# Performance work log

Measured on AMD Instinct MI355X. Metric: run time of the kernel, lower is better.

The kernel has to match this reference:

```python
import jax, jax.numpy as jnp
import numpy as np

NEG = float(-2**32 + 1)  # mask fill value used by the original module
H = 8  # number of heads (matches init kwarg h)


def setup_inputs() -> dict:
    key = jax.random.key(0)
    B, S, D, Q, V = 4, 2048, 512, 64, 64
    ks = jax.random.split(key, 10)
    sc = 1.0 / np.sqrt(D)
    x = jax.random.normal(ks[0], (B, S, D), jnp.float32)
    padding_mask = jax.random.randint(ks[1], (B, S), 0, 2, jnp.int32)
    Wq = jax.random.normal(ks[2], (H * Q, D), jnp.float32) * sc
    bq = jnp.zeros((H * Q,), jnp.float32)
    Wk = jax.random.normal(ks[3], (H * Q, D), jnp.float32) * sc
    bk = jnp.zeros((H * Q,), jnp.float32)
    Wv = jax.random.normal(ks[4], (H * V, D), jnp.float32) * sc
    bv = jnp.zeros((H * V,), jnp.float32)
    Wo = jax.random.normal(ks[5], (D, H * V), jnp.float32) * (1.0 / np.sqrt(H * V))
    bo = jnp.zeros((D,), jnp.float32)
    return {"x": x, "padding_mask": padding_mask, "Wq": Wq, "bq": bq,
            "Wk": Wk, "bk": bk, "Wv": Wv, "bv": bv, "Wo": Wo, "bo": bo}


def reference(x, padding_mask, Wq, bq, Wk, bk, Wv, bv, Wo, bo):
    # stage is hardcoded to 'train' (mask=True in init), so the causal branch runs.
    B, S, D = x.shape
    q_dim = Wq.shape[0] // H
    v_dim = Wv.shape[0] // H

    def split_heads(t, d):
        # torch: cat(chunk(h, dim=-1), dim=0) -> head-major [H*B, S, d]
        return t.reshape(B, S, H, d).transpose(2, 0, 1, 3).reshape(H * B, S, d)

    Qh = split_heads(x @ Wq.T + bq, q_dim)   # [H*B, S, q]
    Kh = split_heads(x @ Wk.T + bk, q_dim)
    Vh = split_heads(x @ Wv.T + bv, v_dim)

    score = jnp.einsum('nsd,ntd->nst', Qh, Kh) / jnp.sqrt(jnp.float32(q_dim))  # [H*B,S,S]
    pre_score = score  # module returns the UNMASKED scores (saved before masking)

    # causal mask (mask=True, stage=='train')
    causal = jnp.tril(jnp.ones((S, S), jnp.float32))
    score = jnp.where(causal > 0, score, NEG)

    # padding mask: built batch-major [B*H,S,S] while score is head-major [H*B,...]
    # -- faithful reproduction of the original ordering quirk.
    pm = jnp.broadcast_to(padding_mask[:, None, None, :], (B, H, S, S)).reshape(B * H, S, S)
    score = jnp.where(pm == 0, NEG, score)

    attn = jax.nn.softmax(score, axis=-1)
    out = jnp.einsum('nst,ntd->nsd', attn, Vh)  # [H*B, S, v]

    # torch: cat(chunk(h, dim=0), dim=-1) -> [B, S, H*v]
    heads = out.reshape(H, B, S, v_dim).transpose(1, 2, 0, 3).reshape(B, S, H * v_dim)
    self_attention = heads @ Wo.T + bo
    return self_attention, pre_score
```

## Files before the change

### kernel.cpp

```cpp
#include <hip/hip_runtime.h>
#include <hip/hip_fp16.h>
#include <math.h>

typedef _Float16 f16;
typedef _Float16 f16x8 __attribute__((ext_vector_type(8)));
typedef _Float16 f16x4 __attribute__((ext_vector_type(4)));
typedef float    f32x4 __attribute__((ext_vector_type(4)));

#define MFMA16(a,b,c) __builtin_amdgcn_mfma_f32_16x16x32_f16(a, b, c, 0, 0, 0)

#define MASKNEG (-6.0e9f)
#define DEADTHR (-1.0e9f)
#define LOG2E   1.44269504088896f

__global__ __launch_bounds__(256) void qkv_gemm(
    const float* __restrict__ x,
    const float* __restrict__ Wq, const float* __restrict__ bq,
    const float* __restrict__ Wk, const float* __restrict__ bk,
    const float* __restrict__ Wv, const float* __restrict__ bv,
    f16* __restrict__ Qws, f16* __restrict__ Kws, f16* __restrict__ Vt)
{
    __shared__ f16 Al[128 * 48];
    __shared__ f16 Wl[64 * 48];

    const int tid = threadIdx.x;
    const int bx  = blockIdx.x;
    const int m0  = blockIdx.y * 128;
    const int widx = bx >> 3;
    const int n0   = (bx & 7) * 64;

    const float* W    = (widx == 0) ? Wq : (widx == 1) ? Wk : Wv;
    const float* bias = (widx == 0) ? bq : (widx == 1) ? bk : bv;
    const float scl  = (widx == 0) ? 0.125f : 1.0f;

    const int wid = tid >> 6, lane = tid & 63;
    const int g = lane >> 4, c = lane & 15;
    const int wm = (wid >> 1) * 64, wn = (wid & 1) * 32;
    const int sr = tid >> 3, sc = tid & 7;

    f32x4 acc[4][2] = {};

    for (int kk = 0; kk < 512; kk += 32) {
        __syncthreads();
        #pragma unroll
        for (int rr = 0; rr < 4; ++rr) {
            int row = sr + rr * 32;
            float4 v = *(const float4*)&x[(size_t)(m0 + row) * 512 + kk + sc * 4];
            f16x4 h4 = {(f16)v.x, (f16)v.y, (f16)v.z, (f16)v.w};
            *(f16x4*)&Al[row * 48 + sc * 4] = h4;
        }
        #pragma unroll
        for (int rr = 0; rr < 2; ++rr) {
            int row = sr + rr * 32;
            float4 v = *(const float4*)&W[(size_t)(n0 + row) * 512 + kk + sc * 4];
            f16x4 h4 = {(f16)v.x, (f16)v.y, (f16)v.z, (f16)v.w};
            *(f16x4*)&Wl[row * 48 + sc * 4] = h4;
        }
        __syncthreads();

        f16x8 b0 = *(const f16x8*)&Wl[(wn +  0 + c) * 48 + g * 8];
        f16x8 b1 = *(const f16x8*)&Wl[(wn + 16 + c) * 48 + g * 8];
        #pragma unroll
        for (int mf = 0; mf < 4; ++mf) {
            f16x8 a = *(const f16x8*)&Al[(wm + mf * 16 + c) * 48 + g * 8];
            acc[mf][0] = MFMA16(a, b0, acc[mf][0]);
            acc[mf][1] = MFMA16(a, b1, acc[mf][1]);
        }
    }

    #pragma unroll
    for (int nf = 0; nf < 2; ++nf) {
        int cc = n0 + wn + nf * 16 + c;
        float bval = bias[cc];
        #pragma unroll
        for (int mf = 0; mf < 4; ++mf) {
            if (widx < 2) {
                f16* outp = (widx == 0) ? Qws : Kws;
                #pragma unroll
                for (int r = 0; r < 4; ++r) {
                    int mrow = m0 + wm + mf * 16 + g * 4 + r;
                    outp[(size_t)mrow * 512 + cc] = (f16)((acc[mf][nf][r] + bval) * scl);
                }
            } else {
                int h  = n0 >> 6;
                int d  = wn + nf * 16 + c;
                int t0 = m0 + wm + mf * 16 + g * 4;
                int b  = t0 >> 11;
                int ts = t0 & 2047;
                int nn = h * 4 + b;
                f16x4 pk = {(f16)(acc[mf][nf][0] + bval), (f16)(acc[mf][nf][1] + bval),
                            (f16)(acc[mf][nf][2] + bval), (f16)(acc[mf][nf][3] + bval)};
                *(f16x4*)&Vt[((size_t)(nn * 64 + d)) * 2048 + ts] = pk;
            }
        }
    }
}

__global__ __launch_bounds__(256) void vsum_kernel(
    const f16* __restrict__ Vt, float* __restrict__ Vsum)
{
    const int row  = blockIdx.x * 4 + (threadIdx.x >> 6);
    const int lane = threadIdx.x & 63;
    const f16* p = Vt + (size_t)row * 2048;
    float s = 0.f;
    #pragma unroll
    for (int i = 0; i < 4; ++i) {
        f16x8 v = *(const f16x8*)&p[i * 512 + lane * 8];
        #pragma unroll
        for (int j = 0; j < 8; ++j) s += (float)v[j];
    }
    #pragma unroll
    for (int off = 1; off < 64; off <<= 1) s += __shfl_xor(s, off, 64);
    if (lane == 0) Vsum[row] = s;
}

__global__ __launch_bounds__(256) void attn_kernel(
    const f16* __restrict__ Qws, const f16* __restrict__ Kws,
    const f16* __restrict__ Vt,  const int* __restrict__ pmask,
    const float* __restrict__ Vsum,
    float* __restrict__ pre_score, f16* __restrict__ attn_out)
{
    __shared__ f16 Kl[64 * 72];
    __shared__ f16 Vl[64 * 72];
    __shared__ f16 Pl[4][32 * 72];
    __shared__ float Bias[2048];

    const int tid = threadIdx.x;
    const int wid = tid >> 6, lane = tid & 63;
    const int g = lane >> 4, c = lane & 15;
    const int qt = blockIdx.x;
    const int n  = blockIdx.y;
    const int h = n >> 2, b = n & 3;
    const int pmrow = n >> 3;
    const int qlo = qt * 64 + wid * 16;
    const int qhi = (31 - qt) * 64 + wid * 16;
    const int qrel = wid * 16 + c;

    {
        const int i0 = tid * 8;
        const int4* p4 = (const int4*)(pmask + pmrow * 2048 + i0);
        int4 m0 = p4[0], m1 = p4[1];
        Bias[i0 + 0] = m0.x ? 0.f : MASKNEG;
        Bias[i0 + 1] = m0.y ? 0.f : MASKNEG;
        Bias[i0 + 2] = m0.z ? 0.f : MASKNEG;
        Bias[i0 + 3] = m0.w ? 0.f : MASKNEG;
        Bias[i0 + 4] = m1.x ? 0.f : MASKNEG;
        Bias[i0 + 5] = m1.y ? 0.f : MASKNEG;
        Bias[i0 + 6] = m1.z ? 0.f : MASKNEG;
        Bias[i0 + 7] = m1.w ? 0.f : MASKNEG;
    }

    f16x8 qf[2][2];
    #pragma unroll
    for (int ks = 0; ks < 2; ++ks) {
        qf[0][ks] = *(const f16x8*)
            &Qws[(size_t)(b * 2048 + qlo + c) * 512 + h * 64 + ks * 32 + g * 8];
        qf[1][ks] = *(const f16x8*)
            &Qws[(size_t)(b * 2048 + qhi + c) * 512 + h * 64 + ks * 32 + g * 8];
    }

    f32x4 o[2][4] = {};
    float mrow[2] = {-INFINITY, -INFINITY};
    float lrow[2] = {0.f, 0.f};

    const int sr = tid >> 3, sc = tid & 7;
    const f16* Kbase = Kws + (size_t)(b * 2048) * 512 + h * 64;
    const f16* Vbase = Vt + (size_t)(n * 64) * 2048;
    float* prow0 = pre_score + ((size_t)n * 2048 + qlo + c) * 2048;
    float* prow1 = pre_score + ((size_t)n * 2048 + qhi + c) * 2048;

    const int stageEnd = 32 - qt;

    uint4 ka0, ka1, va0, va1;
    auto glbload = [&](int kt) {
        ka0 = *(const uint4*)&Kbase[(size_t)(kt * 64 + sr) * 512 + sc * 8];
        ka1 = *(const uint4*)&Kbase[(size_t)(kt * 64 + sr + 32) * 512 + sc * 8];
        va0 = *(const uint4*)&Vbase[(size_t)sr * 2048 + kt * 64 + sc * 8];
        va1 = *(const uint4*)&Vbase[(size_t)(sr + 32) * 2048 + kt * 64 + sc * 8];
    };

    glbload(0);
    for (int kt = 0; kt < stageEnd; ++kt) {
        asm volatile("s_waitcnt lgkmcnt(0)" ::: "memory");
        __builtin_amdgcn_s_barrier();
        *(uint4*)&Kl[sr * 72 + sc * 8]        = ka0;
        *(uint4*)&Kl[(sr + 32) * 72 + sc * 8] = ka1;
        *(uint4*)&Vl[sr * 72 + sc * 8]        = va0;
        *(uint4*)&Vl[(sr + 32) * 72 + sc * 8] = va1;
        asm volatile("s_waitcnt lgkmcnt(0)" ::: "memory");
        __builtin_amdgcn_s_barrier();
        if (kt + 1 < stageEnd) glbload(kt + 1);

        f32x4 s2[2][4] = {};
        #pragma unroll
        for (int kc = 0; kc < 4; ++kc)
            #pragma unroll
            for (int ks = 0; ks < 2; ++ks) {
                f16x8 kf = *(const f16x8*)&Kl[(kc * 16 + c) * 72 + ks * 32 + g * 8];
                s2[0][kc] = MFMA16(kf, qf[0][ks], s2[0][kc]);
                s2[1][kc] = MFMA16(kf, qf[1][ks], s2[1][kc]);
            }

        #pragma unroll
        for (int kc = 0; kc < 4; ++kc) {
            *(f32x4*)&prow0[kt * 64 + kc * 16 + g * 4] = s2[0][kc];
            *(f32x4*)&prow1[kt * 64 + kc * 16 + g * 4] = s2[1][kc];
        }

        f32x4 bi[4];
        #pragma unroll
        for (int kc = 0; kc < 4; ++kc)
            bi[kc] = *(const f32x4*)&Bias[kt * 64 + kc * 16 + g * 4];

        const bool L0 = (kt <= qt);
        const bool bnd0 = (kt == qt), bnd1 = (kt == 31 - qt);

        #pragma unroll
        for (int mi = 0; mi < 2; ++mi) {
            if (mi == 0 && !L0) continue;
            const bool bnd = mi ? bnd1 : bnd0;
            float sl[4][4];
            #pragma unroll
            for (int kc = 0; kc < 4; ++kc)
                #pragma unroll
                for (int r = 0; r < 4; ++r) {
                    float sv = s2[mi][kc][r] + bi[kc][r];
                    int klocal = kc * 16 + g * 4 + r;
                    sl[kc][r] = (bnd && klocal > qrel) ? MASKNEG : sv;
                }
            float rm = sl[0][0];
            #pragma unroll
            for (int kc = 0; kc < 4; ++kc)
                #pragma unroll
                for (int r = 0; r < 4; ++r) rm = fmaxf(rm, sl[kc][r]);
            rm = fmaxf(rm, __shfl_xor(rm, 16, 64));
            rm = fmaxf(rm, __shfl_xor(rm, 32, 64));
            float mn = fmaxf(mrow[mi], rm);
            float alpha = exp2f((mrow[mi] - mn) * LOG2E);
            mrow[mi] = mn;
            float ml2 = mn * LOG2E;
            float rs = 0.f;
            #pragma unroll
            for (int kc = 0; kc < 4; ++kc) {
                f16x4 pk;
                #pragma unroll
                for (int r = 0; r < 4; ++r) {
                    float p = exp2f(fmaf(sl[kc][r], LOG2E, -ml2));
                    rs += p;
                    pk[r] = (f16)p;
                }
                *(f16x4*)&Pl[wid][(mi * 16 + c) * 72 + kc * 16 + g * 4] = pk;
            }
            rs += __shfl_xor(rs, 16, 64);
            rs += __shfl_xor(rs, 32, 64);
            lrow[mi] = lrow[mi] * alpha + rs;
            #pragma unroll
            for (int r = 0; r < 4; ++r) {
                float af = __shfl(alpha, g * 4 + r, 64);
                #pragma unroll
                for (int dn = 0; dn < 4; ++dn) o[mi][dn][r] *= af;
            }
        }
        asm volatile("s_waitcnt lgkmcnt(0)" ::: "memory");

        #pragma unroll
        for (int ks = 0; ks < 2; ++ks) {
            f16x8 pa0, pa1;
            if (L0) pa0 = *(const f16x8*)&Pl[wid][( 0 + c) * 72 + ks * 32 + g * 8];
            pa1 = *(const f16x8*)&Pl[wid][(16 + c) * 72 + ks * 32 + g * 8];
            #pragma unroll
            for (int dn = 0; dn < 4; ++dn) {
                f16x8 vb = *(const f16x8*)&Vl[(dn * 16 + c) * 72 + ks * 32 + g * 8];
                if (L0) o[0][dn] = MFMA16(pa0, vb, o[0][dn]);
                o[1][dn] = MFMA16(pa1, vb, o[1][dn]);
            }
        }
    }

    for (int kt = stageEnd; kt < 32; ++kt) {
        f32x4 s2[2][4] = {};
        #pragma unroll
        for (int kc = 0; kc < 4; ++kc)
            #pragma unroll
            for (int ks = 0; ks < 2; ++ks) {
                f16x8 kf = *(const f16x8*)
                    &Kbase[(size_t)(kt * 64 + kc * 16 + c) * 512 + ks * 32 + g * 8];
                s2[0][kc] = MFMA16(kf, qf[0][ks], s2[0][kc]);
                s2[1][kc] = MFMA16(kf, qf[1][ks], s2[1][kc]);
            }
        #pragma unroll
        for (int kc = 0; kc < 4; ++kc) {
            *(f32x4*)&prow0[kt * 64 + kc * 16 + g * 4] = s2[0][kc];
            *(f32x4*)&prow1[kt * 64 + kc * 16 + g * 4] = s2[1][kc];
        }
    }

    #pragma unroll
    for (int mi = 0; mi < 2; ++mi) {
        int qb = mi ? qhi : qlo;
        #pragma unroll
        for (int r = 0; r < 4; ++r) {
            float lo = __shfl(lrow[mi], g * 4 + r, 64);
            float mo = __shfl(mrow[mi], g * 4 + r, 64);
            int srow = qb + g * 4 + r;
            bool dead = (mo < DEADTHR);
            float inv_l = dead ? 0.f : 1.0f / lo;
            #pragma unroll
            for (int dn = 0; dn < 4; ++dn) {
                float val = dead ? Vsum[n * 64 + dn * 16 + c] * (1.0f / 2048.0f)
                                 : o[mi][dn][r] * inv_l;
                attn_out[(size_t)(b * 2048 + srow) * 512 + h * 64 + dn * 16 + c] = (f16)val;
            }
        }
    }
}

__global__ __launch_bounds__(256) void out_gemm(
    const f16* __restrict__ Aattn, const float* __restrict__ Wo,
    const float* __restrict__ bo, float* __restrict__ outp)
{
    __shared__ f16 Al[128 * 48];
    __shared__ f16 Wl[64 * 48];

    const int tid = threadIdx.x;
    const int n0 = blockIdx.x * 64;
    const int m0 = blockIdx.y * 128;
    const int wid = tid >> 6, lane = tid & 63;
    const int g = lane >> 4, c = lane & 15;
    const int wm = (wid >> 1) * 64, wn = (wid & 1) * 32;

    const int sr4 = tid >> 2, sc4 = tid & 3;
    const int sr8 = tid >> 3, sc8 = tid & 7;

    f32x4 acc[4][2] = {};

    for (int kk = 0; kk < 512; kk += 32) {
        __syncthreads();
        #pragma unroll
        for (int rr = 0; rr < 2; ++rr) {
            int row = sr4 + rr * 64;
            *(uint4*)&Al[row * 48 + sc4 * 8] =
                *(const uint4*)&Aattn[(size_t)(m0 + row) * 512 + kk + sc4 * 8];
        }
        #pragma unroll
        for (int rr = 0; rr < 2; ++rr) {
            int row = sr8 + rr * 32;
            float4 v = *(const float4*)&Wo[(size_t)(n0 + row) * 512 + kk + sc8 * 4];
            f16x4 h4 = {(f16)v.x, (f16)v.y, (f16)v.z, (f16)v.w};
            *(f16x4*)&Wl[row * 48 + sc8 * 4] = h4;
        }
        __syncthreads();

        f16x8 b0 = *(const f16x8*)&Wl[(wn +  0 + c) * 48 + g * 8];
        f16x8 b1 = *(const f16x8*)&Wl[(wn + 16 + c) * 48 + g * 8];
        #pragma unroll
        for (int mf = 0; mf < 4; ++mf) {
            f16x8 a = *(const f16x8*)&Al[(wm + mf * 16 + c) * 48 + g * 8];
            acc[mf][0] = MFMA16(a, b0, acc[mf][0]);
            acc[mf][1] = MFMA16(a, b1, acc[mf][1]);
        }
    }

    #pragma unroll
    for (int nf = 0; nf < 2; ++nf) {
        int cc = n0 + wn + nf * 16 + c;
        float bval = bo[cc];
        #pragma unroll
        for (int mf = 0; mf < 4; ++mf)
            #pragma unroll
            for (int r = 0; r < 4; ++r)
                outp[(size_t)(m0 + wm + mf * 16 + g * 4 + r) * 512 + cc] =
                    acc[mf][nf][r] + bval;
    }
}

extern "C" void kernel_launch(void* const* d_in, const int* in_sizes, int n_in,
                              void* d_out, int out_size, void* d_ws, size_t ws_size,
                              hipStream_t stream)
{
    (void)in_sizes; (void)n_in; (void)out_size; (void)ws_size;

    const float* x  = (const float*)d_in[0];
    const int*   pm = (const int*)  d_in[1];
    const float* Wq = (const float*)d_in[2];
    const float* bq = (const float*)d_in[3];
    const float* Wk = (const float*)d_in[4];
    const float* bk = (const float*)d_in[5];
    const float* Wv = (const float*)d_in[6];
    const float* bv = (const float*)d_in[7];
    const float* Wo = (const float*)d_in[8];
    const float* bo = (const float*)d_in[9];

    float* out = (float*)d_out;
    float* pre = out + (size_t)4 * 2048 * 512;

    f16*   Qws  = (f16*)d_ws;
    f16*   Kws  = Qws + (size_t)8192 * 512;
    f16*   Vt   = Kws + (size_t)8192 * 512;
    f16*   Aat  = Vt  + (size_t)2048 * 2048;
    float* Vsum = (float*)(Aat + (size_t)8192 * 512);

    qkv_gemm   <<<dim3(24, 64), 256, 0, stream>>>(x, Wq, bq, Wk, bk, Wv, bv, Qws, Kws, Vt);
    vsum_kernel<<<dim3(512),    256, 0, stream>>>(Vt, Vsum);
    attn_kernel<<<dim3(16, 32), 256, 0, stream>>>(Qws, Kws, Vt, pm, Vsum, pre, Aat);
    out_gemm   <<<dim3(8, 64),  256, 0, stream>>>(Aat, Wo, bo, out);
}
```

Before: 286.0 us.

## Unify attention tile loops and batch pre-score stores across four key tiles

Merges the causal softmax loop and the score-only tail loop into one loop over all 32 key tiles, so K and V always go through the LDS prefetch pipeline. Each half of the query rows now skips the softmax and PV work once it is past its causal limit. The raw scores are kept in registers as fp16 for four tiles and then written to the fp32 pre_score output together, giving wider contiguous stores. This rounds the returned unmasked scores to fp16 precision, and the extra buffer raises register pressure.

Result: slower. 317.9 us (+11.2%).

```diff
diff --git a/kernel.cpp b/kernel.cpp
--- a/kernel.cpp
+++ b/kernel.cpp
@@ -169,8 +169,6 @@
     float* prow0 = pre_score + ((size_t)n * 2048 + qlo + c) * 2048;
     float* prow1 = pre_score + ((size_t)n * 2048 + qhi + c) * 2048;
 
-    const int stageEnd = 32 - qt;
-
     uint4 ka0, ka1, va0, va1;
     auto glbload = [&](int kt) {
         ka0 = *(const uint4*)&Kbase[(size_t)(kt * 64 + sr) * 512 + sc * 8];
@@ -179,119 +177,127 @@
         va1 = *(const uint4*)&Vbase[(size_t)(sr + 32) * 2048 + kt * 64 + sc * 8];
     };
 
+    f16x4 sbuf[2][4][4];
+
     glbload(0);
-    for (int kt = 0; kt < stageEnd; ++kt) {
-        asm volatile("s_waitcnt lgkmcnt(0)" ::: "memory");
-        __builtin_amdgcn_s_barrier();
-        *(uint4*)&Kl[sr * 72 + sc * 8]        = ka0;
-        *(uint4*)&Kl[(sr + 32) * 72 + sc * 8] = ka1;
-        *(uint4*)&Vl[sr * 72 + sc * 8]        = va0;
-        *(uint4*)&Vl[(sr + 32) * 72 + sc * 8] = va1;
-        asm volatile("s_waitcnt lgkmcnt(0)" ::: "memory");
-        __builtin_amdgcn_s_barrier();
-        if (kt + 1 < stageEnd) glbload(kt + 1);
-
-        f32x4 s2[2][4] = {};
-        #pragma unroll
-        for (int kc = 0; kc < 4; ++kc)
-            #pragma unroll
-            for (int ks = 0; ks < 2; ++ks) {
-                f16x8 kf = *(const f16x8*)&Kl[(kc * 16 + c) * 72 + ks * 32 + g * 8];
-                s2[0][kc] = MFMA16(kf, qf[0][ks], s2[0][kc]);
-                s2[1][kc] = MFMA16(kf, qf[1][ks], s2[1][kc]);
-            }
-
-        #pragma unroll
-        for (int kc = 0; kc < 4; ++kc) {
-            *(f32x4*)&prow0[kt * 64 + kc * 16 + g * 4] = s2[0][kc];
-            *(f32x4*)&prow1[kt * 64 + kc * 16 + g * 4] = s2[1][kc];
-        }
-
-        f32x4 bi[4];
-        #pragma unroll
-        for (int kc = 0; kc < 4; ++kc)
-            bi[kc] = *(const f32x4*)&Bias[kt * 64 + kc * 16 + g * 4];
-
-        const bool L0 = (kt <= qt);
-        const bool bnd0 = (kt == qt), bnd1 = (kt == 31 - qt);
-
-        #pragma unroll
-        for (int mi = 0; mi < 2; ++mi) {
-            if (mi == 0 && !L0) continue;
-            const bool bnd = mi ? bnd1 : bnd0;
-            float sl[4][4];
+    for (int kt0 = 0; kt0 < 32; kt0 += 4) {
+        #pragma unroll
+        for (int j = 0; j < 4; ++j) {
+            const int kt = kt0 + j;
+            asm volatile("s_waitcnt lgkmcnt(0)" ::: "memory");
+            __builtin_amdgcn_s_barrier();
+            *(uint4*)&Kl[sr * 72 + sc * 8]        = ka0;
+            *(uint4*)&Kl[(sr + 32) * 72 + sc * 8] = ka1;
+            *(uint4*)&Vl[sr * 72 + sc * 8]        = va0;
+            *(uint4*)&Vl[(sr + 32) * 72 + sc * 8] = va1;
+            asm volatile("s_waitcnt lgkmcnt(0)" ::: "memory");
+            __builtin_amdgcn_s_barrier();
+            if (kt < 31) glbload(kt + 1);
+
+            f32x4 s2[2][4] = {};
             #pragma unroll
             for (int kc = 0; kc < 4; ++kc)
                 #pragma unroll
-                for (int r = 0; r < 4; ++r) {
-                    float sv = s2[mi][kc][r] + bi[kc][r];
-                    int klocal = kc * 16 + g * 4 + r;
-                    sl[kc][r] = (bnd && klocal > qrel) ? MASKNEG : sv;
-                }
-            float rm = sl[0][0];
+                for (int ks = 0; ks < 2; ++ks) {
+                    f16x8 kf = *(const f16x8*)&Kl[(kc * 16 + c) * 72 + ks * 32 + g * 8];
+                    s2[0][kc] = MFMA16(kf, qf[0][ks], s2[0][kc]);
+                    s2[1][kc] = MFMA16(kf, qf[1][ks], s2[1][kc]);
+                }
+
             #pragma unroll
-            for (int kc = 0; kc < 4; ++kc)
-                #pragma unroll
-                for (int r = 0; r < 4; ++r) rm = fmaxf(rm, sl[kc][r]);
-            rm = fmaxf(rm, __shfl_xor(rm, 16, 64));
-            rm = fmaxf(rm, __shfl_xor(rm, 32, 64));
-            float mn = fmaxf(mrow[mi], rm);
-            float alpha = exp2f((mrow[mi] - mn) * LOG2E);
-            mrow[mi] = mn;
-            float ml2 = mn * LOG2E;
-            float rs = 0.f;
+            for (int mi = 0; mi < 2; ++mi)
+                #pragma unroll
+                for (int kc = 0; kc < 4; ++kc) {
+                    f16x4 hv = {(f16)s2[mi][kc][0], (f16)s2[mi][kc][1],
+                                (f16)s2[mi][kc][2], (f16)s2[mi][kc][3]};
+                    sbuf[mi][j][kc] = hv;
+                }
+
+            const bool L0 = (kt <= qt);
+            const bool L1 = (kt <= 31 - qt);
+            if (L0 || L1) {
+                f32x4 bi[4];
+                #pragma unroll
+                for (int kc = 0; kc < 4; ++kc)
+                    bi[kc] = *(const f32x4*)&Bias[kt * 64 + kc * 16 + g * 4];
+
+                const bool bnd0 = (kt == qt), bnd1 = (kt == 31 - qt);
+                #pragma unroll
+                for (int mi = 0; mi < 2; ++mi) {
+                    if (mi == 0 && !L0) continue;
+                    if (mi == 1 && !L1) continue;
+                    const bool bnd = mi ? bnd1 : bnd0;
+                    float sl[4][4];
+                    #pragma unroll
+                    for (int kc = 0; kc < 4; ++kc)
+                        #pragma unroll
+                        for (int r = 0; r < 4; ++r) {
+                            float sv = s2[mi][kc][r] + bi[kc][r];
+                            int klocal = kc * 16 + g * 4 + r;
+                            sl[kc][r] = (bnd && klocal > qrel) ? MASKNEG : sv;
+                        }
+                    float rm = sl[0][0];
+                    #pragma unroll
+                    for (int kc = 0; kc < 4; ++kc)
+                        #pragma unroll
+                        for (int r = 0; r < 4; ++r) rm = fmaxf(rm, sl[kc][r]);
+                    rm = fmaxf(rm, __shfl_xor(rm, 16, 64));
+                    rm = fmaxf(rm, __shfl_xor(rm, 32, 64));
+                    float mn = fmaxf(mrow[mi], rm);
+                    float alpha = exp2f((mrow[mi] - mn) * LOG2E);
+                    mrow[mi] = mn;
+                    float ml2 = mn * LOG2E;
+                    float rs = 0.f;
+                    #pragma unroll
+                    for (int kc = 0; kc < 4; ++kc) {
+                        f16x4 pk;
+                        #pragma unroll
+                        for (int r = 0; r < 4; ++r) {
+                            float p = exp2f(fmaf(sl[kc][r], LOG2E, -ml2));
+                            rs += p;
+                            pk[r] = (f16)p;
+                        }
+                        *(f16x4*)&Pl[wid][(mi * 16 + c) * 72 + kc * 16 + g * 4] = pk;
+                    }
+                    rs += __shfl_xor(rs, 16, 64);
+                    rs += __shfl_xor(rs, 32, 64);
+                    lrow[mi] = lrow[mi] * alpha + rs;
+                    #pragma unroll
+                    for (int r = 0; r < 4; ++r) {
+                        float af = __shfl(alpha, g * 4 + r, 64);
+                        #pragma unroll
+                        for (int dn = 0; dn < 4; ++dn) o[mi][dn][r] *= af;
+                    }
+                }
+                asm volatile("s_waitcnt lgkmcnt(0)" ::: "memory");
+
+                #pragma unroll
+                for (int ks = 0; ks < 2; ++ks) {
+                    f16x8 pa0, pa1;
+                    if (L0) pa0 = *(const f16x8*)&Pl[wid][( 0 + c) * 72 + ks * 32 + g * 8];
+                    if (L1) pa1 = *(const f16x8*)&Pl[wid][(16 + c) * 72 + ks * 32 + g * 8];
+                    #pragma unroll
+                    for (int dn = 0; dn < 4; ++dn) {
+                        f16x8 vb = *(const f16x8*)&Vl[(dn * 16 + c) * 72 + ks * 32 + g * 8];
+                        if (L0) o[0][dn] = MFMA16(pa0, vb, o[0][dn]);
+                        if (L1) o[1][dn] = MFMA16(pa1, vb, o[1][dn]);
+                    }
+                }
+            }
+        }
+
+        #pragma unroll
+        for (int mi = 0; mi < 2; ++mi) {
+            float* pr = mi ? prow1 : prow0;
             #pragma unroll
-            for (int kc = 0; kc < 4; ++kc) {
-                f16x4 pk;
-                #pragma unroll
-                for (int r = 0; r < 4; ++r) {
-                    float p = exp2f(fmaf(sl[kc][r], LOG2E, -ml2));
-                    rs += p;
-                    pk[r] = (f16)p;
-                }
-                *(f16x4*)&Pl[wid][(mi * 16 + c) * 72 + kc * 16 + g * 4] = pk;
-            }
-            rs += __shfl_xor(rs, 16, 64);
-            rs += __shfl_xor(rs, 32, 64);
-            lrow[mi] = lrow[mi] * alpha + rs;
-            #pragma unroll
-            for (int r = 0; r < 4; ++r) {
-                float af = __shfl(alpha, g * 4 + r, 64);
-                #pragma unroll
-                for (int dn = 0; dn < 4; ++dn) o[mi][dn][r] *= af;
-            }
-        }
-        asm volatile("s_waitcnt lgkmcnt(0)" ::: "memory");
-
-        #pragma unroll
-        for (int ks = 0; ks < 2; ++ks) {
-            f16x8 pa0, pa1;
-            if (L0) pa0 = *(const f16x8*)&Pl[wid][( 0 + c) * 72 + ks * 32 + g * 8];
-            pa1 = *(const f16x8*)&Pl[wid][(16 + c) * 72 + ks * 32 + g * 8];
-            #pragma unroll
-            for (int dn = 0; dn < 4; ++dn) {
-                f16x8 vb = *(const f16x8*)&Vl[(dn * 16 + c) * 72 + ks * 32 + g * 8];
-                if (L0) o[0][dn] = MFMA16(pa0, vb, o[0][dn]);
-                o[1][dn] = MFMA16(pa1, vb, o[1][dn]);
-            }
-        }
-    }
-
-    for (int kt = stageEnd; kt < 32; ++kt) {
-        f32x4 s2[2][4] = {};
-        #pragma unroll
-        for (int kc = 0; kc < 4; ++kc)
-            #pragma unroll
-            for (int ks = 0; ks < 2; ++ks) {
-                f16x8 kf = *(const f16x8*)
-                    &Kbase[(size_t)(kt * 64 + kc * 16 + c) * 512 + ks * 32 + g * 8];
-                s2[0][kc] = MFMA16(kf, qf[0][ks], s2[0][kc]);
-                s2[1][kc] = MFMA16(kf, qf[1][ks], s2[1][kc]);
-            }
-        #pragma unroll
-        for (int kc = 0; kc < 4; ++kc) {
-            *(f32x4*)&prow0[kt * 64 + kc * 16 + g * 4] = s2[0][kc];
-            *(f32x4*)&prow1[kt * 64 + kc * 16 + g * 4] = s2[1][kc];
+            for (int j = 0; j < 4; ++j)
+                #pragma unroll
+                for (int kc = 0; kc < 4; ++kc) {
+                    f16x4 hv = sbuf[mi][j][kc];
+                    f32x4 v = {(float)hv[0], (float)hv[1],
+                               (float)hv[2], (float)hv[3]};
+                    *(f32x4*)&pr[(size_t)(kt0 + j) * 64 + kc * 16 + g * 4] = v;
+                }
         }
     }
 
```
